# Optimization experiments

Measured on AMD Instinct MI355X. Metric: run time of the kernel, lower is better.

## Reference

```python
import jax, jax.numpy as jnp
import numpy as np

N_AGENTS = 50000  # number of batch elements (agents); fixed num_segments
N_NEIGHBORS = 1600000  # total ragged neighbors flattened (avg degree 32)
STATE_DIM = 64
PHI_HID = 64
PHI_OUT = 64
RHO_HID = 64
ACT_DIM = 2


def setup_inputs() -> dict:
    key = jax.random.key(0)
    ks = jax.random.split(key, 6)
    s = lambda fan_in: 1.0 / np.sqrt(fan_in)
    neighbors = jax.random.normal(ks[0], (N_NEIGHBORS, STATE_DIM), dtype=jnp.float32)
    phi_w1 = jax.random.normal(ks[1], (STATE_DIM, PHI_HID), dtype=jnp.float32) * s(STATE_DIM)
    phi_b1 = jnp.zeros((PHI_HID,), dtype=jnp.float32)
    phi_w2 = jax.random.normal(ks[2], (PHI_HID, PHI_OUT), dtype=jnp.float32) * s(PHI_HID)
    phi_b2 = jnp.zeros((PHI_OUT,), dtype=jnp.float32)
    rho_w1 = jax.random.normal(ks[3], (PHI_OUT, RHO_HID), dtype=jnp.float32) * s(PHI_OUT)
    rho_b1 = jnp.zeros((RHO_HID,), dtype=jnp.float32)
    rho_w2 = jax.random.normal(ks[4], (RHO_HID, ACT_DIM), dtype=jnp.float32) * s(RHO_HID)
    rho_b2 = jnp.zeros((ACT_DIM,), dtype=jnp.float32)
    segment_ids = jnp.sort(jax.random.randint(ks[5], (N_NEIGHBORS,), 0, N_AGENTS, dtype=jnp.int32))
    return {
        "neighbors": neighbors,
        "phi_w1": phi_w1, "phi_b1": phi_b1, "phi_w2": phi_w2, "phi_b2": phi_b2,
        "rho_w1": rho_w1, "rho_b1": rho_b1, "rho_w2": rho_w2, "rho_b2": rho_b2,
        "segment_ids": segment_ids,
    }


def reference(neighbors, phi_w1, phi_b1, phi_w2, phi_b2,
              rho_w1, rho_b1, rho_w2, rho_b2, segment_ids):
    # phi MLP applied to every neighbor feature (vectorized over the flat ragged axis)
    h = jax.nn.relu(neighbors @ phi_w1 + phi_b1)          # [N_NEIGHBORS, PHI_HID]
    h = h @ phi_w2 + phi_b2                               # [N_NEIGHBORS, PHI_OUT]
    # per-agent sum over variable-length neighbor sets (the Python double loop in torch)
    summ = jax.ops.segment_sum(h, segment_ids, num_segments=N_AGENTS)  # [N_AGENTS, PHI_OUT]
    # rho MLP on pooled features
    r = jax.nn.relu(summ @ rho_w1 + rho_b1)               # [N_AGENTS, RHO_HID]
    return r @ rho_w2 + rho_b2                            # [N_AGENTS, ACT_DIM]
```

## Files before the change

kernel.cpp:

```cpp
#include <hip/hip_runtime.h>
#include <hip/hip_bf16.h>

#define N_AGENTS 50000
#define N_NEI    1600000
#define ROWS     128
#define PHI_BLOCKS (N_NEI / ROWS)

typedef __bf16 bf16_t;
typedef __attribute__((ext_vector_type(8))) __bf16 bf16x8;
typedef __attribute__((ext_vector_type(4))) float  f32x4;

#define SO 66

#define WS_SUMM   0
#define WS_CNT    3200000
#define WS_WC     3250000
#define WS_BC     3254096
#define WS_W1PK   3254160
#define WS_ZERO_F 3250000

__global__ __launch_bounds__(256) void prep_kernel(
    const float* __restrict__ w1g, const float* __restrict__ w2g,
    const float* __restrict__ b2g, const float* __restrict__ rw1g,
    unsigned short* __restrict__ w1pack, float* __restrict__ Wc,
    float* __restrict__ bc)
{
  const int tid = threadIdx.x;
  if (blockIdx.x == 0) {
    for (int i = tid; i < 4096; i += 256) {
      int k = i >> 6, n = i & 63;
      int tn = n >> 4, kb = k >> 5;
      int l  = (n & 15) + 16 * ((k >> 3) & 3);
      int j  = k & 7;
      bf16_t bv = (bf16_t)w1g[i];
      w1pack[((tn * 2 + kb) * 64 + l) * 8 + j] = *(unsigned short*)&bv;
    }
  } else {
    for (int i = tid; i < 4096; i += 256) {
      int h = i >> 6, n = i & 63;
      float s = 0.f;
      #pragma unroll 8
      for (int o = 0; o < 64; ++o) s = fmaf(w2g[h * 64 + o], rw1g[o * 64 + n], s);
      Wc[i] = s;
    }
    if (tid < 64) {
      float s = 0.f;
      for (int o = 0; o < 64; ++o) s = fmaf(b2g[o], rw1g[o * 64 + tid], s);
      bc[tid] = s;
    }
  }
}

__global__ __launch_bounds__(256, 4) void phi_kernel(
    const float* __restrict__ nb, const float* __restrict__ b1g,
    const int* __restrict__ seg, const unsigned short* __restrict__ w1pack,
    float* __restrict__ summH1, float* __restrict__ cnt)
{
  __shared__ __align__(16) union {
    struct {
      bf16_t Afr[16 * 64 * 8];
      bf16_t Wfr[8 * 64 * 8];
    } s;
    float outb[ROWS * SO];
  } u;
  __shared__ float biasf[64];
  __shared__ int sid[ROWS];

  const int tid  = threadIdx.x;
  const int w    = tid >> 6;
  const int lane = tid & 63;
  const int m16  = lane & 15;
  const int q    = lane >> 4;
  const long base = (long)blockIdx.x * ROWS;

  if (tid < ROWS) sid[tid] = seg[base + tid];
  if (tid < 64)  biasf[tid] = b1g[tid];

  #pragma unroll
  for (int c = 0; c < 2; ++c) {
    int chunk = w * 2 + c;
    __builtin_amdgcn_global_load_lds(
        (const __attribute__((address_space(1))) void*)(w1pack + chunk * 512 + lane * 8),
        (__attribute__((address_space(3))) void*)(&u.s.Wfr[chunk * 512]),
        16, 0, 0);
  }

  #pragma unroll
  for (int it = 0; it < 4; ++it) {
    int tile = 2 * w + (it >> 1), kb = it & 1;
    int row = tile * 16 + m16;
    const float4* g = (const float4*)(nb + (base + row) * 64 + kb * 32 + q * 8);
    float4 v0 = g[0], v1 = g[1];
    bf16x8 p = { (bf16_t)v0.x, (bf16_t)v0.y, (bf16_t)v0.z, (bf16_t)v0.w,
                 (bf16_t)v1.x, (bf16_t)v1.y, (bf16_t)v1.z, (bf16_t)v1.w };
    *(bf16x8*)&u.s.Afr[((tile * 2 + kb) * 64 + lane) * 8] = p;
  }
  __syncthreads();

  bf16x8 afr[2][2], bfr[4][2];
  #pragma unroll
  for (int tm = 0; tm < 2; ++tm)
    #pragma unroll
    for (int kb = 0; kb < 2; ++kb)
      afr[tm][kb] = *(const bf16x8*)&u.s.Afr[(((2 * w + tm) * 2 + kb) * 64 + lane) * 8];
  #pragma unroll
  for (int tn = 0; tn < 4; ++tn)
    #pragma unroll
    for (int kb = 0; kb < 2; ++kb)
      bfr[tn][kb] = *(const bf16x8*)&u.s.Wfr[((tn * 2 + kb) * 64 + lane) * 8];

  f32x4 acc[2][4];
  #pragma unroll
  for (int tm = 0; tm < 2; ++tm)
    #pragma unroll
    for (int tn = 0; tn < 4; ++tn) {
      f32x4 a = {0.f, 0.f, 0.f, 0.f};
      a = __builtin_amdgcn_mfma_f32_16x16x32_bf16(afr[tm][0], bfr[tn][0], a, 0, 0, 0);
      a = __builtin_amdgcn_mfma_f32_16x16x32_bf16(afr[tm][1], bfr[tn][1], a, 0, 0, 0);
      acc[tm][tn] = a;
    }
  __syncthreads();

  const int rb = w * 32;
  #pragma unroll
  for (int tm = 0; tm < 2; ++tm)
    #pragma unroll
    for (int tn = 0; tn < 4; ++tn) {
      float bv = biasf[tn * 16 + m16];
      #pragma unroll
      for (int i = 0; i < 4; ++i)
        u.outb[(rb + tm * 16 + q * 4 + i) * SO + tn * 16 + m16] =
            fmaxf(acc[tm][tn][i] + bv, 0.f);
    }

  float racc = 0.f;
  int runlen = 0;
  for (int r = rb; r < rb + 32; ++r) {
    racc += u.outb[r * SO + lane];
    ++runlen;
    int sr = sid[r];
    if (r == rb + 31 || sid[r + 1] != sr) {
      atomicAdd(summH1 + (long)sr * 64 + lane, racc);
      if (lane == 0) atomicAdd(cnt + sr, (float)runlen);
      racc = 0.f;
      runlen = 0;
    }
  }
}

__global__ __launch_bounds__(256) void rho_kernel(
    const float* __restrict__ summH1, const float* __restrict__ cnt,
    const float* __restrict__ Wc, const float* __restrict__ bc,
    const float* __restrict__ rb1g, const float* __restrict__ rw2g,
    const float* __restrict__ rb2g, float* __restrict__ out)
{
  __shared__ float sW[64 * 64];
  __shared__ float sbc[64], sb1[64], sw2[128], sb2[2];
  const int tid = threadIdx.x;
  for (int i = tid; i < 4096; i += 256) sW[i] = Wc[i];
  if (tid < 64)  { sbc[tid] = bc[tid]; sb1[tid] = rb1g[tid]; }
  if (tid < 128) sw2[tid] = rw2g[tid];
  if (tid < 2)   sb2[tid] = rb2g[tid];
  __syncthreads();

  int a = blockIdx.x * 256 + tid;
  if (a >= N_AGENTS) return;

  float x[64];
  const float4* xr = (const float4*)(summH1 + (long)a * 64);
  #pragma unroll
  for (int i = 0; i < 16; ++i) {
    float4 v = xr[i];
    x[4 * i] = v.x; x[4 * i + 1] = v.y; x[4 * i + 2] = v.z; x[4 * i + 3] = v.w;
  }
  float c = cnt[a];

  float o0 = sb2[0], o1 = sb2[1];
  for (int n = 0; n < 64; ++n) {
    float a0 = fmaf(c, sbc[n], sb1[n]), a1 = 0.f, a2 = 0.f, a3 = 0.f;
    #pragma unroll
    for (int k = 0; k < 64; k += 4) {
      a0 = fmaf(x[k],     sW[(k)     * 64 + n], a0);
      a1 = fmaf(x[k + 1], sW[(k + 1) * 64 + n], a1);
      a2 = fmaf(x[k + 2], sW[(k + 2) * 64 + n], a2);
      a3 = fmaf(x[k + 3], sW[(k + 3) * 64 + n], a3);
    }
    float h = fmaxf((a0 + a1) + (a2 + a3), 0.f);
    o0 = fmaf(h, sw2[2 * n],     o0);
    o1 = fmaf(h, sw2[2 * n + 1], o1);
  }
  *(float2*)(out + (long)a * 2) = make_float2(o0, o1);
}

extern "C" void kernel_launch(void* const* d_in, const int* in_sizes, int n_in,
                              void* d_out, int out_size, void* d_ws, size_t ws_size,
                              hipStream_t stream) {
  const float* neighbors = (const float*)d_in[0];
  const float* phi_w1    = (const float*)d_in[1];
  const float* phi_b1    = (const float*)d_in[2];
  const float* phi_w2    = (const float*)d_in[3];
  const float* phi_b2    = (const float*)d_in[4];
  const float* rho_w1    = (const float*)d_in[5];
  const float* rho_b1    = (const float*)d_in[6];
  const float* rho_w2    = (const float*)d_in[7];
  const float* rho_b2    = (const float*)d_in[8];
  const int*   seg       = (const int*)d_in[9];
  float* out = (float*)d_out;

  float* ws     = (float*)d_ws;
  float* summH1 = ws + WS_SUMM;
  float* cntp   = ws + WS_CNT;
  float* Wc     = ws + WS_WC;
  float* bc     = ws + WS_BC;
  unsigned short* w1pack = (unsigned short*)(ws + WS_W1PK);

  hipMemsetAsync(ws, 0, (size_t)WS_ZERO_F * sizeof(float), stream);
  prep_kernel<<<2, 256, 0, stream>>>(phi_w1, phi_w2, phi_b2, rho_w1,
                                     w1pack, Wc, bc);
  phi_kernel<<<PHI_BLOCKS, 256, 0, stream>>>(neighbors, phi_b1, seg, w1pack,
                                             summH1, cntp);
  rho_kernel<<<(N_AGENTS + 255) / 256, 256, 0, stream>>>(summH1, cntp, Wc, bc,
                                                         rho_b1, rho_w2, rho_b2, out);
}
```

Before: 628.9 us.

## Hoist neighbor loads ahead of LDS setup and fold weight-combine prep into rho

In phi_kernel, all global loads of neighbor rows, segment ids and bias are issued up front into registers, before the weight LDS copy and the shared-memory writes, so more memory requests are in flight at once. The Wc/bc weight-combination matmul moves out of prep_kernel and into every rho_kernel block, which shrinks prep to a single block. The trade-off is that each of the 196 rho blocks now recomputes a 64x64x64 product from global memory, and phi holds more registers, which may lower occupancy.

Result: no change. 626.5 us (-0.4%).

```diff
diff --git a/kernel.cpp b/kernel.cpp
--- a/kernel.cpp
+++ b/kernel.cpp
@@ -14,40 +14,20 @@
 
 #define WS_SUMM   0
 #define WS_CNT    3200000
-#define WS_WC     3250000
-#define WS_BC     3254096
-#define WS_W1PK   3254160
+#define WS_W1PK   3250000
 #define WS_ZERO_F 3250000
 
 __global__ __launch_bounds__(256) void prep_kernel(
-    const float* __restrict__ w1g, const float* __restrict__ w2g,
-    const float* __restrict__ b2g, const float* __restrict__ rw1g,
-    unsigned short* __restrict__ w1pack, float* __restrict__ Wc,
-    float* __restrict__ bc)
+    const float* __restrict__ w1g, unsigned short* __restrict__ w1pack)
 {
   const int tid = threadIdx.x;
-  if (blockIdx.x == 0) {
-    for (int i = tid; i < 4096; i += 256) {
-      int k = i >> 6, n = i & 63;
-      int tn = n >> 4, kb = k >> 5;
-      int l  = (n & 15) + 16 * ((k >> 3) & 3);
-      int j  = k & 7;
-      bf16_t bv = (bf16_t)w1g[i];
-      w1pack[((tn * 2 + kb) * 64 + l) * 8 + j] = *(unsigned short*)&bv;
-    }
-  } else {
-    for (int i = tid; i < 4096; i += 256) {
-      int h = i >> 6, n = i & 63;
-      float s = 0.f;
-      #pragma unroll 8
-      for (int o = 0; o < 64; ++o) s = fmaf(w2g[h * 64 + o], rw1g[o * 64 + n], s);
-      Wc[i] = s;
-    }
-    if (tid < 64) {
-      float s = 0.f;
-      for (int o = 0; o < 64; ++o) s = fmaf(b2g[o], rw1g[o * 64 + tid], s);
-      bc[tid] = s;
-    }
+  for (int i = tid; i < 4096; i += 256) {
+    int k = i >> 6, n = i & 63;
+    int tn = n >> 4, kb = k >> 5;
+    int l  = (n & 15) + 16 * ((k >> 3) & 3);
+    int j  = k & 7;
+    bf16_t bv = (bf16_t)w1g[i];
+    w1pack[((tn * 2 + kb) * 64 + l) * 8 + j] = *(unsigned short*)&bv;
   }
 }
 
@@ -73,8 +53,17 @@
   const int q    = lane >> 4;
   const long base = (long)blockIdx.x * ROWS;
 
-  if (tid < ROWS) sid[tid] = seg[base + tid];
-  if (tid < 64)  biasf[tid] = b1g[tid];
+  float4 xv[4][2];
+  #pragma unroll
+  for (int it = 0; it < 4; ++it) {
+    int tile = 2 * w + (it >> 1), kb = it & 1;
+    int row = tile * 16 + m16;
+    const float4* g = (const float4*)(nb + (base + row) * 64 + kb * 32 + q * 8);
+    xv[it][0] = g[0];
+    xv[it][1] = g[1];
+  }
+  int   sv  = (tid < ROWS) ? seg[base + tid] : 0;
+  float bvv = (tid < 64)   ? b1g[tid]        : 0.f;
 
   #pragma unroll
   for (int c = 0; c < 2; ++c) {
@@ -85,12 +74,12 @@
         16, 0, 0);
   }
 
+  if (tid < ROWS) sid[tid] = sv;
+  if (tid < 64)  biasf[tid] = bvv;
   #pragma unroll
   for (int it = 0; it < 4; ++it) {
     int tile = 2 * w + (it >> 1), kb = it & 1;
-    int row = tile * 16 + m16;
-    const float4* g = (const float4*)(nb + (base + row) * 64 + kb * 32 + q * 8);
-    float4 v0 = g[0], v1 = g[1];
+    float4 v0 = xv[it][0], v1 = xv[it][1];
     bf16x8 p = { (bf16_t)v0.x, (bf16_t)v0.y, (bf16_t)v0.z, (bf16_t)v0.w,
                  (bf16_t)v1.x, (bf16_t)v1.y, (bf16_t)v1.z, (bf16_t)v1.w };
     *(bf16x8*)&u.s.Afr[((tile * 2 + kb) * 64 + lane) * 8] = p;
@@ -150,15 +139,29 @@
 
 __global__ __launch_bounds__(256) void rho_kernel(
     const float* __restrict__ summH1, const float* __restrict__ cnt,
-    const float* __restrict__ Wc, const float* __restrict__ bc,
-    const float* __restrict__ rb1g, const float* __restrict__ rw2g,
-    const float* __restrict__ rb2g, float* __restrict__ out)
+    const float* __restrict__ w2g,  const float* __restrict__ b2g,
+    const float* __restrict__ rw1g, const float* __restrict__ rb1g,
+    const float* __restrict__ rw2g, const float* __restrict__ rb2g,
+    float* __restrict__ out)
 {
   __shared__ float sW[64 * 64];
   __shared__ float sbc[64], sb1[64], sw2[128], sb2[2];
   const int tid = threadIdx.x;
-  for (int i = tid; i < 4096; i += 256) sW[i] = Wc[i];
-  if (tid < 64)  { sbc[tid] = bc[tid]; sb1[tid] = rb1g[tid]; }
+
+  for (int i = tid; i < 4096; i += 256) {
+    int h = i >> 6, n = i & 63;
+    float s = 0.f;
+    #pragma unroll 8
+    for (int o = 0; o < 64; ++o) s = fmaf(w2g[h * 64 + o], rw1g[o * 64 + n], s);
+    sW[i] = s;
+  }
+  if (tid < 64) {
+    float s = 0.f;
+    #pragma unroll 8
+    for (int o = 0; o < 64; ++o) s = fmaf(b2g[o], rw1g[o * 64 + tid], s);
+    sbc[tid] = s;
+    sb1[tid] = rb1g[tid];
+  }
   if (tid < 128) sw2[tid] = rw2g[tid];
   if (tid < 2)   sb2[tid] = rb2g[tid];
   __syncthreads();
@@ -210,15 +213,12 @@
   float* ws     = (float*)d_ws;
   float* summH1 = ws + WS_SUMM;
   float* cntp   = ws + WS_CNT;
-  float* Wc     = ws + WS_WC;
-  float* bc     = ws + WS_BC;
   unsigned short* w1pack = (unsigned short*)(ws + WS_W1PK);
 
   hipMemsetAsync(ws, 0, (size_t)WS_ZERO_F * sizeof(float), stream);
-  prep_kernel<<<2, 256, 0, stream>>>(phi_w1, phi_w2, phi_b2, rho_w1,
-                                     w1pack, Wc, bc);
+  prep_kernel<<<1, 256, 0, stream>>>(phi_w1, w1pack);
   phi_kernel<<<PHI_BLOCKS, 256, 0, stream>>>(neighbors, phi_b1, seg, w1pack,
                                              summH1, cntp);
-  rho_kernel<<<(N_AGENTS + 255) / 256, 256, 0, stream>>>(summH1, cntp, Wc, bc,
-                                                         rho_b1, rho_w2, rho_b2, out);
-}
+  rho_kernel<<<(N_AGENTS + 255) / 256, 256, 0, stream>>>(
+      summH1, cntp, phi_w2, phi_b2, rho_w1, rho_b1, rho_w2, rho_b2, out);
+}
```
